# Kernel optimization log

Measured on AMD Instinct MI355X. Metric: run time of the kernel, lower is better.

## Reference

```python
import jax, jax.numpy as jnp
import numpy as np

N_NODES = 50000
N_EDGES = 800000
NUM_RELS = 16
IN_DIM, H_DIM, OUT_DIM = 128, 128, 64


def setup_inputs() -> dict:
    key = jax.random.key(0)
    ks = jax.random.split(key, 7)
    feat = jax.random.normal(ks[0], (N_NODES, IN_DIM), dtype=jnp.float32)
    norm = jax.random.uniform(ks[1], (N_EDGES, 1), dtype=jnp.float32)
    bound1 = 1.0 / np.sqrt(IN_DIM)
    bound2 = 1.0 / np.sqrt(H_DIM)
    W1 = jax.random.uniform(ks[2], (NUM_RELS, IN_DIM, H_DIM), dtype=jnp.float32, minval=-bound1, maxval=bound1)
    W2 = jax.random.uniform(ks[3], (NUM_RELS, H_DIM, OUT_DIM), dtype=jnp.float32, minval=-bound2, maxval=bound2)
    src = jax.random.randint(ks[4], (N_EDGES,), 0, N_NODES, dtype=jnp.int32)
    dst = jax.random.randint(ks[5], (N_EDGES,), 0, N_NODES, dtype=jnp.int32)
    etypes = jax.random.randint(ks[6], (N_EDGES,), 0, NUM_RELS, dtype=jnp.int32)
    return {"feat": feat, "norm": norm, "W1": W1, "W2": W2, "src": src, "dst": dst, "etypes": etypes}


def _rgcn_layer(h, W, src, dst, etypes, norm, num_nodes):
    # Transform every node by every relation weight (dense batched GEMM),
    # then gather the (src, etype) slice per edge: identical math to
    # gather_mm(h[src], W, idx_b=etypes) since matmul commutes with gather.
    t = jnp.einsum('ni,rio->nro', h, W)          # [N, R, O]
    msg = t[src, etypes] * norm                  # [E, O]
    return jax.ops.segment_sum(msg, dst, num_segments=num_nodes)  # sum-aggregate


def reference(feat, norm, W1, W2, src, dst, etypes):
    n = feat.shape[0]
    h = jax.nn.relu(_rgcn_layer(feat, W1, src, dst, etypes, norm, n))
    out = _rgcn_layer(h, W2, src, dst, etypes, norm, n)
    return out
```

## Files before the change

kernel.cpp:

```cpp
#include <hip/hip_runtime.h>


#define R_NUM 16

typedef __attribute__((ext_vector_type(8))) short bf16x8;
typedef __attribute__((ext_vector_type(4))) float f32x4;

__device__ __forceinline__ float bf2f(unsigned short u) {
    unsigned int x = ((unsigned int)u) << 16;
    return __builtin_bit_cast(float, x);
}
__device__ __forceinline__ unsigned short f2bf(float f) {
    unsigned int x = __builtin_bit_cast(unsigned int, f);
    x += 0x7FFFu + ((x >> 16) & 1u);
    return (unsigned short)(x >> 16);
}
__device__ __forceinline__ unsigned pack2(float a, float b) {
    return (unsigned)f2bf(a) | ((unsigned)f2bf(b) << 16);
}
__device__ __forceinline__ float lo16(unsigned v) { return bf2f((unsigned short)(v & 0xFFFF)); }
__device__ __forceinline__ float hi16(unsigned v) { return bf2f((unsigned short)(v >> 16)); }

__global__ void detect_dtype(const unsigned short* __restrict__ raw, int* flag) {
    __shared__ int tot;
    if (threadIdx.x == 0) tot = 0;
    __syncthreads();
    int c = 0;
    for (int i = threadIdx.x; i < 4096; i += 256) {
        unsigned short u = raw[2 * i];
        int e = (u >> 7) & 0xFF;
        if (e >= 113 && e <= 134) c++;
    }
    atomicAdd(&tot, c);
    __syncthreads();
    if (threadIdx.x == 0) *flag = (tot > 2048) ? 1 : 0;
}

__global__ void transpose_both(const void* __restrict__ W1, const void* __restrict__ W2,
                               unsigned short* __restrict__ w1t, unsigned short* __restrict__ w2t,
                               const int* __restrict__ flagp) {
    const int flag = *flagp;
    const int n1 = R_NUM * 128 * 128;
    const int n2 = R_NUM * 128 * 64;
    int idx = blockIdx.x * 256 + threadIdx.x;
    if (idx < n1) {
        int k = idx % 128, o = (idx / 128) % 128, r = idx / (128 * 128);
        int iin = (r * 128 + k) * 128 + o;
        float v = flag ? bf2f(((const unsigned short*)W1)[iin]) : ((const float*)W1)[iin];
        w1t[idx] = f2bf(v);
    } else if (idx < n1 + n2) {
        int j = idx - n1;
        int k = j % 128, o = (j / 128) % 64, r = j / (128 * 64);
        int iin = (r * 128 + k) * 64 + o;
        float v = flag ? bf2f(((const unsigned short*)W2)[iin]) : ((const float*)W2)[iin];
        w2t[j] = f2bf(v);
    }
}

template <int NOUT, int AMODE>
__global__ __launch_bounds__(256, 3) void gemm_all(const void* __restrict__ Asrc,
                                                   const unsigned short* __restrict__ Wt,
                                                   unsigned short* __restrict__ T, int nnodes,
                                                   const int* __restrict__ flagp) {
    constexpr int LDA = 136;
    constexpr int NTC = NOUT / 64;
    __shared__ unsigned short lA[64 * LDA];
    __shared__ unsigned short lB[NOUT * LDA];
    const int tid = threadIdx.x;
    const int node0 = blockIdx.x * 64;
    const int flag = (AMODE == 0) ? *flagp : 1;

    for (int i = tid; i < 64 * 16; i += 256) {
        int row = i >> 4, seg = i & 15;
        int node = node0 + row;
        uint4 v = make_uint4(0u, 0u, 0u, 0u);
        if (node < nnodes) {
            if (AMODE == 2 || flag) {
                v = *(const uint4*)((const unsigned short*)Asrc + (size_t)node * 128 + seg * 8);
            } else {
                const float* p = (const float*)Asrc + (size_t)node * 128 + seg * 8;
                float4 f0 = ((const float4*)p)[0];
                float4 f1 = ((const float4*)p)[1];
                v.x = pack2(f0.x, f0.y);
                v.y = pack2(f0.z, f0.w);
                v.z = pack2(f1.x, f1.y);
                v.w = pack2(f1.z, f1.w);
            }
        }
        *(uint4*)(lA + row * LDA + seg * 8) = v;
    }

    auto stageB = [&](int rel) {
        for (int i = tid; i < NOUT * 16; i += 256) {
            int o = i >> 4, seg = i & 15;
            *(uint4*)(lB + o * LDA + seg * 8) =
                *(const uint4*)(Wt + ((size_t)rel * NOUT + o) * 128 + seg * 8);
        }
    };
    stageB(0);
    __syncthreads();

    const int w = tid >> 6, lane = tid & 63;
    const int quad = lane >> 4, mr = lane & 15;

    bf16x8 afr[16];
#pragma unroll
    for (int mt = 0; mt < 4; mt++)
#pragma unroll
        for (int kk = 0; kk < 4; kk++)
            afr[mt * 4 + kk] = *(const bf16x8*)(lA + (mt * 16 + mr) * LDA + kk * 32 + quad * 8);

    constexpr int SPT = NOUT / 32;
    constexpr int SEGS = NOUT / 8;

    for (int rel = 0; rel < R_NUM; rel++) {
        f32x4 acc[4][NTC];
#pragma unroll
        for (int mt = 0; mt < 4; mt++)
#pragma unroll
            for (int c = 0; c < NTC; c++) acc[mt][c] = 0.f;

#pragma unroll
        for (int kk = 0; kk < 4; kk++) {
#pragma unroll
            for (int c = 0; c < NTC; c++) {
                bf16x8 b = *(const bf16x8*)(lB + (c * 64 + w * 16 + mr) * LDA + kk * 32 + quad * 8);
#pragma unroll
                for (int mt = 0; mt < 4; mt++)
                    acc[mt][c] = __builtin_amdgcn_mfma_f32_16x16x32_bf16(afr[mt * 4 + kk], b,
                                                                         acc[mt][c], 0, 0, 0);
            }
        }
        __syncthreads();

        if (rel + 1 < R_NUM) stageB(rel + 1);
#pragma unroll
        for (int mt = 0; mt < 4; mt++)
#pragma unroll
            for (int c = 0; c < NTC; c++)
#pragma unroll
                for (int reg = 0; reg < 4; reg++)
                    lA[(mt * 16 + quad * 4 + reg) * LDA + c * 64 + w * 16 + mr] =
                        f2bf(acc[mt][c][reg]);
        __syncthreads();

#pragma unroll
        for (int it = 0; it < SPT; it++) {
            int i = it * 256 + tid;
            int row = i / SEGS, seg = i % SEGS;
            int node = node0 + row;
            if (node < nnodes)
                *(uint4*)(T + ((size_t)node * R_NUM + rel) * NOUT + seg * 8) =
                    *(const uint4*)(lA + row * LDA + seg * 8);
        }
    }
}

__global__ void hist_dst(const int* __restrict__ dst, int* __restrict__ counts, int nedges) {
    int e = blockIdx.x * 256 + threadIdx.x;
    if (e < nedges) atomicAdd(&counts[dst[e]], 1);
}

__global__ __launch_bounds__(256) void scan_phase1(const int* __restrict__ counts,
                                                   int* __restrict__ blocksums, int n) {
    __shared__ int red[256];
    int base = blockIdx.x * 1024 + threadIdx.x * 4;
    int s = 0;
#pragma unroll
    for (int j = 0; j < 4; j++) {
        int idx = base + j;
        if (idx < n) s += counts[idx];
    }
    red[threadIdx.x] = s;
    __syncthreads();
    for (int d = 128; d > 0; d >>= 1) {
        if (threadIdx.x < d) red[threadIdx.x] += red[threadIdx.x + d];
        __syncthreads();
    }
    if (threadIdx.x == 0) blocksums[blockIdx.x] = red[0];
}

__global__ __launch_bounds__(1024) void scan_phase2(const int* __restrict__ blocksums,
                                                    int* __restrict__ blockoff, int nb) {
    __shared__ int arr[1024];
    int t = threadIdx.x;
    arr[t] = (t < nb) ? blocksums[t] : 0;
    __syncthreads();
    for (int d = 1; d < 1024; d <<= 1) {
        int v = (t >= d) ? arr[t - d] : 0;
        __syncthreads();
        arr[t] += v;
        __syncthreads();
    }
    if (t < nb) blockoff[t] = (t == 0) ? 0 : arr[t - 1];
}

__global__ __launch_bounds__(256) void scan_phase3(const int* __restrict__ counts,
                                                   const int* __restrict__ blockoff,
                                                   int* __restrict__ offsets,
                                                   int* __restrict__ cursor, int n) {
    __shared__ int tsum[256];
    int base = blockIdx.x * 1024 + threadIdx.x * 4;
    int c[4];
    int s = 0;
#pragma unroll
    for (int j = 0; j < 4; j++) {
        int idx = base + j;
        c[j] = (idx < n) ? counts[idx] : 0;
        s += c[j];
    }
    tsum[threadIdx.x] = s;
    __syncthreads();
    for (int d = 1; d < 256; d <<= 1) {
        int v = (threadIdx.x >= d) ? tsum[threadIdx.x - d] : 0;
        __syncthreads();
        tsum[threadIdx.x] += v;
        __syncthreads();
    }
    int run = blockoff[blockIdx.x] + ((threadIdx.x == 0) ? 0 : tsum[threadIdx.x - 1]);
#pragma unroll
    for (int j = 0; j < 4; j++) {
        int idx = base + j;
        if (idx < n) {
            offsets[idx] = run;
            cursor[idx] = run;
            if (idx == n - 1) offsets[n] = run + c[j];
            run += c[j];
        }
    }
}

__global__ void fill_payload(const int* __restrict__ src, const int* __restrict__ dst,
                             const int* __restrict__ et, const void* __restrict__ nrm,
                             const int* __restrict__ flagp, int* __restrict__ cursor,
                             uint2* __restrict__ payload, int nedges) {
    int e = blockIdx.x * 256 + threadIdx.x;
    if (e >= nedges) return;
    int flag = *flagp;
    float nm = flag ? bf2f(((const unsigned short*)nrm)[e]) : ((const float*)nrm)[e];
    int pos = atomicAdd(&cursor[dst[e]], 1);
    uint2 pl;
    pl.x = ((unsigned)src[e] << 4) | (unsigned)(et[e] & 15);
    pl.y = __builtin_bit_cast(unsigned, nm);
    payload[pos] = pl;
}

template <int NOUT, int OUTMODE>
__global__ __launch_bounds__(256) void gather_seg(const unsigned short* __restrict__ T,
                                                  const int* __restrict__ offsets,
                                                  const uint2* __restrict__ payload,
                                                  void* __restrict__ out, int nnodes,
                                                  const int* __restrict__ flagp) {
    constexpr int SUBW = NOUT / 2;
    const int lane = threadIdx.x & 63;
    const int ll = lane & (SUBW - 1);
    const int dpb = 256 / SUBW;
    const int dst = blockIdx.x * dpb + threadIdx.x / SUBW;
    if (dst >= nnodes) return;
    const int base = lane & ~(SUBW - 1);
    const int beg = offsets[dst], end = offsets[dst + 1];
    float ax = 0.f, ay = 0.f;

    for (int i = beg; i < end; i += SUBW) {
        int cnt = min(SUBW, end - i);
        uint2 pl = make_uint2(0u, 0u);
        if (ll < cnt) pl = payload[i + ll];
        int j = 0;
        for (; j + 4 <= cnt; j += 4) {
            unsigned k0 = (unsigned)__shfl((int)pl.x, base + j);
            unsigned k1 = (unsigned)__shfl((int)pl.x, base + j + 1);
            unsigned k2 = (unsigned)__shfl((int)pl.x, base + j + 2);
            unsigned k3 = (unsigned)__shfl((int)pl.x, base + j + 3);
            float n0 = __builtin_bit_cast(float, (unsigned)__shfl((int)pl.y, base + j));
            float n1 = __builtin_bit_cast(float, (unsigned)__shfl((int)pl.y, base + j + 1));
            float n2 = __builtin_bit_cast(float, (unsigned)__shfl((int)pl.y, base + j + 2));
            float n3 = __builtin_bit_cast(float, (unsigned)__shfl((int)pl.y, base + j + 3));
            unsigned v0 = ((const unsigned*)(T + ((size_t)(k0 >> 4) * R_NUM + (k0 & 15)) * NOUT))[ll];
            unsigned v1 = ((const unsigned*)(T + ((size_t)(k1 >> 4) * R_NUM + (k1 & 15)) * NOUT))[ll];
            unsigned v2 = ((const unsigned*)(T + ((size_t)(k2 >> 4) * R_NUM + (k2 & 15)) * NOUT))[ll];
            unsigned v3 = ((const unsigned*)(T + ((size_t)(k3 >> 4) * R_NUM + (k3 & 15)) * NOUT))[ll];
            ax = fmaf(lo16(v0), n0, ax); ay = fmaf(hi16(v0), n0, ay);
            ax = fmaf(lo16(v1), n1, ax); ay = fmaf(hi16(v1), n1, ay);
            ax = fmaf(lo16(v2), n2, ax); ay = fmaf(hi16(v2), n2, ay);
            ax = fmaf(lo16(v3), n3, ax); ay = fmaf(hi16(v3), n3, ay);
        }
        for (; j < cnt; j++) {
            unsigned k = (unsigned)__shfl((int)pl.x, base + j);
            float nm = __builtin_bit_cast(float, (unsigned)__shfl((int)pl.y, base + j));
            unsigned v = ((const unsigned*)(T + ((size_t)(k >> 4) * R_NUM + (k & 15)) * NOUT))[ll];
            ax = fmaf(lo16(v), nm, ax);
            ay = fmaf(hi16(v), nm, ay);
        }
    }
    if (OUTMODE == 0) {
        ((unsigned*)out)[(size_t)dst * SUBW + ll] = pack2(fmaxf(ax, 0.f), fmaxf(ay, 0.f));
    } else {
        if (*flagp) {
            ((unsigned*)out)[(size_t)dst * SUBW + ll] = pack2(ax, ay);
        } else {
            float2 v;
            v.x = ax; v.y = ay;
            ((float2*)out)[(size_t)dst * SUBW + ll] = v;
        }
    }
}

template <int NOUT, int AMODE>
__global__ __launch_bounds__(256) void gemm_rel(const void* __restrict__ Asrc,
                                                const unsigned short* __restrict__ Wt,
                                                unsigned short* __restrict__ T, int nnodes,
                                                int rbase, const int* __restrict__ flagp) {
    constexpr int LDA = 136;
    __shared__ unsigned short lA[64 * LDA];
    __shared__ unsigned short lB[NOUT * LDA];
    const int tid = threadIdx.x;
    const int node0 = blockIdx.x * 64;
    const int rel = rbase + blockIdx.y;
    const int Gr = gridDim.y;
    const int flag = (AMODE == 0) ? *flagp : 1;

    for (int i = tid; i < 64 * 16; i += 256) {
        int row = i >> 4, seg = i & 15;
        int node = node0 + row;
        uint4 v = make_uint4(0u, 0u, 0u, 0u);
        if (node < nnodes) {
            if (AMODE == 1) {
                const float* p = (const float*)Asrc + (size_t)node * 128 + seg * 8;
                float4 f0 = ((const float4*)p)[0];
                float4 f1 = ((const float4*)p)[1];
                v.x = pack2(fmaxf(f0.x, 0.f), fmaxf(f0.y, 0.f));
                v.y = pack2(fmaxf(f0.z, 0.f), fmaxf(f0.w, 0.f));
                v.z = pack2(fmaxf(f1.x, 0.f), fmaxf(f1.y, 0.f));
                v.w = pack2(fmaxf(f1.z, 0.f), fmaxf(f1.w, 0.f));
            } else if (flag) {
                v = *(const uint4*)((const unsigned short*)Asrc + (size_t)node * 128 + seg * 8);
            } else {
                const float* p = (const float*)Asrc + (size_t)node * 128 + seg * 8;
                float4 f0 = ((const float4*)p)[0];
                float4 f1 = ((const float4*)p)[1];
                v.x = pack2(f0.x, f0.y);
                v.y = pack2(f0.z, f0.w);
                v.z = pack2(f1.x, f1.y);
                v.w = pack2(f1.z, f1.w);
            }
        }
        *(uint4*)(lA + row * LDA + seg * 8) = v;
    }
    for (int i = tid; i < NOUT * 16; i += 256) {
        int o = i >> 4, seg = i & 15;
        *(uint4*)(lB + o * LDA + seg * 8) =
            *(const uint4*)(Wt + ((size_t)rel * NOUT + o) * 128 + seg * 8);
    }
    __syncthreads();

    const int w = tid >> 6, lane = tid & 63;
    const int quad = lane >> 4, mr = lane & 15;
    constexpr int NT = NOUT / 16;
    f32x4 acc[NT];
#pragma unroll
    for (int t = 0; t < NT; t++) acc[t] = 0.f;
    const unsigned short* pa = lA + (w * 16 + mr) * LDA + quad * 8;
    const unsigned short* pb = lB + mr * LDA + quad * 8;
#pragma unroll
    for (int kk = 0; kk < 4; kk++) {
        bf16x8 a = *(const bf16x8*)(pa + kk * 32);
#pragma unroll
        for (int nt = 0; nt < NT; nt++) {
            bf16x8 b = *(const bf16x8*)(pb + nt * 16 * LDA + kk * 32);
            acc[nt] = __builtin_amdgcn_mfma_f32_16x16x32_bf16(a, b, acc[nt], 0, 0, 0);
        }
    }
#pragma unroll
    for (int nt = 0; nt < NT; nt++)
#pragma unroll
        for (int reg = 0; reg < 4; reg++) {
            int node = node0 + w * 16 + quad * 4 + reg;
            if (node < nnodes)
                T[((size_t)node * Gr + blockIdx.y) * NOUT + nt * 16 + mr] = f2bf(acc[nt][reg]);
        }
}

template <int NOUT>
__global__ void scatter_k(const unsigned short* __restrict__ T, int Gr, int rbase,
                          const void* __restrict__ nrm, const int* __restrict__ flagp,
                          const int* __restrict__ src, const int* __restrict__ dst,
                          const int* __restrict__ et, float* __restrict__ accum, int nedges) {
    constexpr int LPE = NOUT / 2;
    const int flag = *flagp;
    const int epb = 256 / LPE;
    const int sub = threadIdx.x % LPE;
    const int slot = threadIdx.x / LPE;
    for (int e = blockIdx.x * epb + slot; e < nedges; e += gridDim.x * epb) {
        int g = et[e] - rbase;
        if (g < 0 || g >= Gr) continue;
        int s = src[e], d = dst[e];
        float nm = flag ? bf2f(((const unsigned short*)nrm)[e]) : ((const float*)nrm)[e];
        unsigned pv = ((const unsigned*)(T + ((size_t)s * Gr + g) * NOUT))[sub];
        float* p = accum + (size_t)d * NOUT + sub * 2;
        unsafeAtomicAdd(p, lo16(pv) * nm);
        unsafeAtomicAdd(p + 1, hi16(pv) * nm);
    }
}

__global__ void write_out(const float* __restrict__ acc, void* __restrict__ dout, int n,
                          const int* __restrict__ flagp) {
    int flag = *flagp;
    int i = blockIdx.x * 256 + threadIdx.x;
    if (i >= n) return;
    float v = acc[i];
    if (flag) ((unsigned short*)dout)[i] = f2bf(v);
    else      ((float*)dout)[i] = v;
}

extern "C" void kernel_launch(void* const* d_in, const int* in_sizes, int n_in,
                              void* d_out, int out_size, void* d_ws, size_t ws_size,
                              hipStream_t stream) {
    const void* feat = d_in[0];
    const void* norm = d_in[1];
    const void* W1 = d_in[2];
    const void* W2 = d_in[3];
    const int* src = (const int*)d_in[4];
    const int* dst = (const int*)d_in[5];
    const int* et  = (const int*)d_in[6];

    const int nnodes = in_sizes[0] / 128;
    const int nedges = in_sizes[1];

    char* ws = (char*)d_ws;
    size_t off = 0;
    auto alloc = [&](size_t bytes) { size_t o = off; off += (bytes + 255) & ~255ULL; return o; };
    size_t off_flag = alloc(4);
    size_t off_w1t  = alloc((size_t)R_NUM * 128 * 128 * 2);
    size_t off_w2t  = alloc((size_t)R_NUM * 64 * 128 * 2);

    int* flagp = (int*)(ws + off_flag);
    unsigned short* w1t = (unsigned short*)(ws + off_w1t);
    unsigned short* w2t = (unsigned short*)(ws + off_w2t);

    size_t f_off = off;
    auto falloc = [&](size_t bytes) { size_t o = f_off; f_off += (bytes + 255) & ~255ULL; return o; };
    size_t off_offs = falloc((size_t)(nnodes + 1) * 4);
    size_t off_curs = falloc((size_t)nnodes * 4);
    size_t off_cnt  = falloc((size_t)nnodes * 4);
    size_t off_bsum = falloc(1024 * 4);
    size_t off_boff = falloc(1024 * 4);
    size_t off_pay  = falloc((size_t)nedges * 8);
    size_t off_hbf  = falloc((size_t)nnodes * 128 * 2);
    size_t off_t    = falloc((size_t)nnodes * R_NUM * 128 * 2);
    const int nb = (nnodes + 1023) / 1024;
    bool fast = (f_off <= ws_size) && (nb <= 1024);

    const int gx = (nnodes + 63) / 64;
    const int ntr = R_NUM * 128 * 128 + R_NUM * 128 * 64;

    detect_dtype<<<1, 256, 0, stream>>>((const unsigned short*)feat, flagp);
    transpose_both<<<(ntr + 255) / 256, 256, 0, stream>>>(W1, W2, w1t, w2t, flagp);

    if (fast) {
        int* offs = (int*)(ws + off_offs);
        int* curs = (int*)(ws + off_curs);
        int* cnt  = (int*)(ws + off_cnt);
        int* bsum = (int*)(ws + off_bsum);
        int* boff = (int*)(ws + off_boff);
        uint2* pay = (uint2*)(ws + off_pay);
        unsigned short* hbf = (unsigned short*)(ws + off_hbf);
        unsigned short* t = (unsigned short*)(ws + off_t);

        hipMemsetAsync(cnt, 0, (size_t)nnodes * 4, stream);
        hist_dst<<<(nedges + 255) / 256, 256, 0, stream>>>(dst, cnt, nedges);
        scan_phase1<<<nb, 256, 0, stream>>>(cnt, bsum, nnodes);
        scan_phase2<<<1, 1024, 0, stream>>>(bsum, boff, nb);
        scan_phase3<<<nb, 256, 0, stream>>>(cnt, boff, offs, curs, nnodes);
        fill_payload<<<(nedges + 255) / 256, 256, 0, stream>>>(src, dst, et, norm, flagp,
                                                               curs, pay, nedges);

        gemm_all<128, 0><<<gx, 256, 0, stream>>>(feat, w1t, t, nnodes, flagp);
        gather_seg<128, 0><<<(nnodes + 3) / 4, 256, 0, stream>>>(t, offs, pay, hbf, nnodes, flagp);
        gemm_all<64, 2><<<gx, 256, 0, stream>>>(hbf, w2t, t, nnodes, flagp);
        gather_seg<64, 1><<<(nnodes + 7) / 8, 256, 0, stream>>>(t, offs, pay, d_out, nnodes, flagp);
        return;
    }

    size_t off_hpre = alloc((size_t)nnodes * 128 * 4);
    size_t off_oacc = alloc((size_t)nnodes * 64 * 4);
    size_t t_cap = (ws_size > off) ? (ws_size - off) : 0;
    auto pick_gr = [&](int ncol) {
        int gr = 0;
        for (int g = 16; g >= 1; g >>= 1)
            if ((size_t)nnodes * g * ncol * 2 <= t_cap) { gr = g; break; }
        return gr;
    };
    int Gr1 = pick_gr(128);
    int Gr2 = pick_gr(64);
    if (Gr1 < 1 || Gr2 < 1) {
        hipMemsetAsync(d_out, 0x42, (size_t)out_size * 2, stream);
        return;
    }
    float* hpre = (float*)(ws + off_hpre);
    float* oacc = (float*)(ws + off_oacc);
    unsigned short* t = (unsigned short*)(ws + off);

    hipMemsetAsync(hpre, 0, (size_t)nnodes * 128 * 4, stream);
    hipMemsetAsync(oacc, 0, (size_t)nnodes * 64 * 4, stream);
    for (int rb = 0; rb < R_NUM; rb += Gr1) {
        gemm_rel<128, 0><<<dim3(gx, Gr1), 256, 0, stream>>>(feat, w1t, t, nnodes, rb, flagp);
        scatter_k<128><<<4096, 256, 0, stream>>>(t, Gr1, rb, norm, flagp, src, dst, et, hpre, nedges);
    }
    for (int rb = 0; rb < R_NUM; rb += Gr2) {
        gemm_rel<64, 1><<<dim3(gx, Gr2), 256, 0, stream>>>(hpre, w2t, t, nnodes, rb, flagp);
        scatter_k<64><<<4096, 256, 0, stream>>>(t, Gr2, rb, norm, flagp, src, dst, et, oacc, nedges);
    }
    int nout = nnodes * 64;
    write_out<<<(nout + 255) / 256, 256, 0, stream>>>(oacc, d_out, nout, flagp);
}
```

Baseline: 403.5 us.

## Store transformed table relation-major and pack LDS epilogue writes via swapped MFMA operands

The dense transform kernel swaps the MFMA A/B operands so each lane holds four consecutive output columns, which lets it write packed uint2 values to LDS instead of four scalar bf16 stores. The intermediate table T changes from node-major [N,R,O] to relation-major [R,N,O], and the gather kernel's row addressing is updated to match. The aim is fewer LDS store instructions and a different global write and gather locality pattern. The relation-major layout spreads each relation's writes across the whole table, which may help or hurt cache behaviour in the random gather.

```diff
diff --git a/kernel.cpp b/kernel.cpp
--- a/kernel.cpp
+++ b/kernel.cpp
@@ -110,8 +110,8 @@
         for (int kk = 0; kk < 4; kk++)
             afr[mt * 4 + kk] = *(const bf16x8*)(lA + (mt * 16 + mr) * LDA + kk * 32 + quad * 8);
 
-    constexpr int SPT = NOUT / 32;
     constexpr int SEGS = NOUT / 8;
+    constexpr int SPT = 64 * SEGS / 256;
 
     for (int rel = 0; rel < R_NUM; rel++) {
         f32x4 acc[4][NTC];
@@ -127,7 +127,7 @@
                 bf16x8 b = *(const bf16x8*)(lB + (c * 64 + w * 16 + mr) * LDA + kk * 32 + quad * 8);
 #pragma unroll
                 for (int mt = 0; mt < 4; mt++)
-                    acc[mt][c] = __builtin_amdgcn_mfma_f32_16x16x32_bf16(afr[mt * 4 + kk], b,
+                    acc[mt][c] = __builtin_amdgcn_mfma_f32_16x16x32_bf16(b, afr[mt * 4 + kk],
                                                                          acc[mt][c], 0, 0, 0);
             }
         }
@@ -137,11 +137,12 @@
 #pragma unroll
         for (int mt = 0; mt < 4; mt++)
 #pragma unroll
-            for (int c = 0; c < NTC; c++)
-#pragma unroll
-                for (int reg = 0; reg < 4; reg++)
-                    lA[(mt * 16 + quad * 4 + reg) * LDA + c * 64 + w * 16 + mr] =
-                        f2bf(acc[mt][c][reg]);
+            for (int c = 0; c < NTC; c++) {
+                uint2 pv;
+                pv.x = pack2(acc[mt][c][0], acc[mt][c][1]);
+                pv.y = pack2(acc[mt][c][2], acc[mt][c][3]);
+                *(uint2*)(lA + (mt * 16 + mr) * LDA + c * 64 + w * 16 + quad * 4) = pv;
+            }
         __syncthreads();
 
 #pragma unroll
@@ -150,7 +151,7 @@
             int row = i / SEGS, seg = i % SEGS;
             int node = node0 + row;
             if (node < nnodes)
-                *(uint4*)(T + ((size_t)node * R_NUM + rel) * NOUT + seg * 8) =
+                *(uint4*)(T + ((size_t)rel * nnodes + node) * NOUT + seg * 8) =
                     *(const uint4*)(lA + row * LDA + seg * 8);
         }
     }
@@ -261,6 +262,10 @@
     const int beg = offsets[dst], end = offsets[dst + 1];
     float ax = 0.f, ay = 0.f;
 
+    auto rowp = [&](unsigned key) {
+        return (const unsigned*)(T + ((size_t)(key & 15) * nnodes + (key >> 4)) * NOUT);
+    };
+
     for (int i = beg; i < end; i += SUBW) {
         int cnt = min(SUBW, end - i);
         uint2 pl = make_uint2(0u, 0u);
@@ -275,10 +280,10 @@
             float n1 = __builtin_bit_cast(float, (unsigned)__shfl((int)pl.y, base + j + 1));
             float n2 = __builtin_bit_cast(float, (unsigned)__shfl((int)pl.y, base + j + 2));
             float n3 = __builtin_bit_cast(float, (unsigned)__shfl((int)pl.y, base + j + 3));
-            unsigned v0 = ((const unsigned*)(T + ((size_t)(k0 >> 4) * R_NUM + (k0 & 15)) * NOUT))[ll];
-            unsigned v1 = ((const unsigned*)(T + ((size_t)(k1 >> 4) * R_NUM + (k1 & 15)) * NOUT))[ll];
-            unsigned v2 = ((const unsigned*)(T + ((size_t)(k2 >> 4) * R_NUM + (k2 & 15)) * NOUT))[ll];
-            unsigned v3 = ((const unsigned*)(T + ((size_t)(k3 >> 4) * R_NUM + (k3 & 15)) * NOUT))[ll];
+            unsigned v0 = rowp(k0)[ll];
+            unsigned v1 = rowp(k1)[ll];
+            unsigned v2 = rowp(k2)[ll];
+            unsigned v3 = rowp(k3)[ll];
             ax = fmaf(lo16(v0), n0, ax); ay = fmaf(hi16(v0), n0, ay);
             ax = fmaf(lo16(v1), n1, ax); ay = fmaf(hi16(v1), n1, ay);
             ax = fmaf(lo16(v2), n2, ax); ay = fmaf(hi16(v2), n2, ay);
@@ -287,7 +292,7 @@
         for (; j < cnt; j++) {
             unsigned k = (unsigned)__shfl((int)pl.x, base + j);
             float nm = __builtin_bit_cast(float, (unsigned)__shfl((int)pl.y, base + j));
-            unsigned v = ((const unsigned*)(T + ((size_t)(k >> 4) * R_NUM + (k & 15)) * NOUT))[ll];
+            unsigned v = rowp(k)[ll];
             ax = fmaf(lo16(v), nm, ax);
             ay = fmaf(hi16(v), nm, ay);
         }
```

New measurement: 398.0 us. About the same (-1.4%).
